# Kernel optimization log

Hardware: AMD Instinct MI355X
Metric: run time of the kernel (lower is better)

The kernel has to match this reference:

```python
import jax, jax.numpy as jnp
import numpy as np

INF_NUMBER = 1.0e12
ZERO_TOL = 1e-9
NEG_SLOPE = 0.2

B, G, N = 16, 128, 512
P, E, K, F = 4, 1, 3, 128


def setup_inputs() -> dict:
    key = jax.random.key(0)
    k1, k2, k3, k4, k5, k6, k7 = jax.random.split(key, 7)
    x = jax.random.normal(k1, (B, G, N), dtype=jnp.float32)
    u = jax.random.uniform(k2, (B, E, N, N), dtype=jnp.float32)
    S = jnp.where(u < 0.1, u, 0.0)
    std = 1.0 / np.sqrt(G * P)
    W = jax.random.uniform(k3, (P, E, G, G), minval=-std, maxval=std, dtype=jnp.float32)
    mixer = jax.random.uniform(k4, (P, E, 2 * F), minval=-std, maxval=std, dtype=jnp.float32)
    h = jax.random.uniform(k5, (P, F, E, K, G), minval=-std, maxval=std, dtype=jnp.float32)
    b = jax.random.uniform(k6, (F, 1), minval=-std, maxval=std, dtype=jnp.float32)
    return {"x": x, "S": S, "W": W, "mixer": mixer, "h": h, "b": b}


def _attention_gso(x, W, S):
    # x: (B,G,N); W: (P,E,G,G); S: (B,E,N,N)
    # Wx = W @ x_query : (B,P,E,G,N)
    Wx = jnp.einsum('pegh,bhn->bpegn', W, x)
    # xWx = x_key @ Wx : (B,P,E,N,N)  (x_key[b,m,g] = x[b,g,m])
    xWx = jnp.einsum('bgm,bpegn->bpemn', x, Wx)
    eij = jax.nn.leaky_relu(xWx, negative_slope=NEG_SLOPE)
    # edge mask from |S| summed over edge features: (B,1,1,N,N)
    mask = (jnp.sum(jnp.abs(S), axis=1) > ZERO_TOL).astype(x.dtype)[:, None, None]
    scores = eij * mask - (1.0 - mask) * INF_NUMBER
    aij = jax.nn.softmax(scores, axis=-1) * mask
    return aij  # (B,P,E,N,N)


def reference(x, S, W, mixer, h, b):
    # mixer is declared by the torch module but unused in key-query mode
    aij = _attention_gso(x, W, S)  # (B,P,E,N,N)
    # K-hop taps: z[k] = x @ aij^k, broadcast over (P,E)
    xk = jnp.broadcast_to(x[:, None, None], (B, P, E, G, N))
    taps = [xk]
    for _ in range(1, K):
        xk = jnp.einsum('bpegn,bpenm->bpegm', xk, aij)
        taps.append(xk)
    z = jnp.stack(taps, axis=3)  # (B,P,E,K,G,N)
    # filter GEMM: contract over (E,K,G) -> (B,P,F,N)
    y = jnp.einsum('bpekgn,pfekg->bpfn', z, h) + b  # b: (F,1) broadcasts
    # concatenate heads: relu then (B, P*F, N)
    y = jax.nn.relu(y)
    y = jnp.transpose(y, (0, 3, 1, 2)).reshape(B, N, P * F)
    return jnp.transpose(y, (0, 2, 1))
```

## Files before the change

### kernel.cpp

```cpp
#include <hip/hip_runtime.h>

#define Bx 16
#define Gx 128
#define Nx 512
#define Px 4
#define Kx 3
#define Fx 128
#define NEG_SLOPE 0.2f
#define ZERO_TOL 1e-9f
#define BIGF 1.0e30f

typedef unsigned short u16;
typedef unsigned int u32;
typedef __bf16 v8bf __attribute__((ext_vector_type(8)));
typedef _Float16 v8hf __attribute__((ext_vector_type(8)));
typedef float v4f __attribute__((ext_vector_type(4)));

__device__ __forceinline__ u16 f2b(float f) {
  union { float f; u32 u; } v; v.f = f;
  u32 r = (v.u + 0x7fffu + ((v.u >> 16) & 1u)) >> 16;
  return (u16)r;
}
__device__ __forceinline__ u16 f2h(float f) {
  union { _Float16 h; u16 u; } v; v.h = (_Float16)f;
  return v.u;
}

#define G2L16(gsrc, ldst)                                                     \
  __builtin_amdgcn_global_load_lds(                                           \
      (const __attribute__((address_space(1))) void*)(gsrc),                  \
      (__attribute__((address_space(3))) void*)(ldst), 16, 0, 0)

__global__ __launch_bounds__(256) void prep_kernel(const float* __restrict__ S,
                                                   const float* __restrict__ x,
                                                   const float* __restrict__ W,
                                                   const float* __restrict__ h,
                                                   u32* __restrict__ mb,
                                                   u16* __restrict__ xb,
                                                   u16* __restrict__ xTb,
                                                   u16* __restrict__ xT16,
                                                   u16* __restrict__ w16,
                                                   u16* __restrict__ Hb) {
  const int blk = blockIdx.x;
  const int tid = threadIdx.x;
  __shared__ float t[32][33];
  if (blk < 512) {
    const int wi = blk * 256 + tid;
    const float4* S4 = (const float4*)S;
    u32 bits = 0;
#pragma unroll
    for (int q = 0; q < 8; q++) {
      float4 v = S4[(size_t)wi * 8 + q];
      bits |= (fabsf(v.x) > ZERO_TOL ? 1u : 0u) << (q * 4);
      bits |= (fabsf(v.y) > ZERO_TOL ? 2u : 0u) << (q * 4);
      bits |= (fabsf(v.z) > ZERO_TOL ? 4u : 0u) << (q * 4);
      bits |= (fabsf(v.w) > ZERO_TOL ? 8u : 0u) << (q * 4);
    }
    mb[wi] = bits;
  } else if (blk < 1536) {
    const int idx = blk - 512;
    const int b = idx >> 6, g0 = ((idx >> 4) & 3) * 32, n0 = (idx & 15) * 32;
    const int r = tid >> 3, c4 = (tid & 7) * 4;
    const float* xp = x + (size_t)b * Gx * Nx;
    float4 v = *(const float4*)&xp[(g0 + r) * Nx + n0 + c4];
    ushort4 o;
    o.x = f2b(v.x); o.y = f2b(v.y); o.z = f2b(v.z); o.w = f2b(v.w);
    *(ushort4*)&xb[(size_t)b * Gx * Nx + (g0 + r) * Nx + n0 + c4] = o;
    t[r][c4 + 0] = v.x; t[r][c4 + 1] = v.y; t[r][c4 + 2] = v.z; t[r][c4 + 3] = v.w;
    __syncthreads();
    float tv[4] = {t[c4 + 0][r], t[c4 + 1][r], t[c4 + 2][r], t[c4 + 3][r]};
    ushort4 ob, oh;
    ob.x = f2b(tv[0]); oh.x = f2h(tv[0]);
    ob.y = f2b(tv[1]); oh.y = f2h(tv[1]);
    ob.z = f2b(tv[2]); oh.z = f2h(tv[2]);
    ob.w = f2b(tv[3]); oh.w = f2h(tv[3]);
    size_t off = (size_t)b * Nx * Gx + (size_t)(n0 + r) * Gx + g0 + c4;
    *(ushort4*)&xTb[off] = ob;
    *(ushort4*)&xT16[off] = oh;
  } else if (blk < 1600) {
    int i4 = ((blk - 1536) * 256 + tid) * 4;
    float4 v = *(const float4*)&W[i4];
    ushort4 o;
    o.x = f2h(v.x); o.y = f2h(v.y); o.z = f2h(v.z); o.w = f2h(v.w);
    *(ushort4*)&w16[i4] = o;
  } else {
    int i4 = ((blk - 1600) * 256 + tid) * 4;
    float4 v = *(const float4*)&h[i4];
    ushort4 o;
    o.x = f2b(v.x); o.y = f2b(v.y); o.z = f2b(v.z); o.w = f2b(v.w);
    *(ushort4*)&Hb[i4] = o;
  }
}

__global__ __launch_bounds__(256) void wxt16_kernel(const u16* __restrict__ xT16,
                                                    const u16* __restrict__ w16,
                                                    u16* __restrict__ WxT16) {
  __shared__ __align__(16) char smem[49152];
  constexpr int OB = 16384;
  const int bp = blockIdx.x, b = bp >> 2, p = bp & 3;
  const int rt = blockIdx.y;
  const int tid = threadIdx.x;
  const int w = tid >> 6, l = tid & 63;
  const int wr = w >> 1, wc = w & 1;
  const int lr = l & 15, ks = l >> 4;

  const u16* Ap = xT16 + ((size_t)b * Nx + rt * 64) * Gx;
  const u16* Bp = w16 + (size_t)p * Gx * Gx;
#pragma unroll
  for (int it = 0; it < 4; it++) {
    int chunk = it * 256 + w * 64 + l;
    int r = chunk >> 4, kq = l & 15;
    int kg = (kq ^ (r & 15)) * 8;
    G2L16(Ap + (size_t)r * Gx + kg, smem + it * 4096 + w * 1024);
  }
#pragma unroll
  for (int it = 0; it < 8; it++) {
    int chunk = it * 256 + w * 64 + l;
    int r = chunk >> 4, kq = l & 15;
    int kg = (kq ^ (r & 15)) * 8;
    G2L16(Bp + (size_t)r * Gx + kg, smem + OB + it * 4096 + w * 1024);
  }
  __syncthreads();

  v4f acc[2][4];
#pragma unroll
  for (int fr = 0; fr < 2; fr++)
#pragma unroll
    for (int fc = 0; fc < 4; fc++) acc[fr][fc] = (v4f){0.f, 0.f, 0.f, 0.f};

#pragma unroll
  for (int t = 0; t < 4; t++) {
    int kk = t * 4 + ks;
    v8hf ah[2];
#pragma unroll
    for (int fr = 0; fr < 2; fr++) {
      int ra = wr * 32 + fr * 16 + lr;
      ah[fr] = *(const v8hf*)(smem + ra * 256 + ((kk ^ (ra & 15)) * 16));
    }
#pragma unroll
    for (int fc = 0; fc < 4; fc++) {
      int rb = wc * 64 + fc * 16 + lr;
      v8hf bh = *(const v8hf*)(smem + OB + rb * 256 + ((kk ^ (rb & 15)) * 16));
#pragma unroll
      for (int fr = 0; fr < 2; fr++)
        acc[fr][fc] = __builtin_amdgcn_mfma_f32_16x16x32_f16(ah[fr], bh, acc[fr][fc], 0, 0, 0);
    }
  }

  u16* op = WxT16 + (size_t)bp * Nx * Gx;
#pragma unroll
  for (int fr = 0; fr < 2; fr++)
#pragma unroll
    for (int fc = 0; fc < 4; fc++) {
      int n = rt * 64 + wr * 32 + fr * 16 + ks * 4;
      int g = wc * 64 + fc * 16 + lr;
#pragma unroll
      for (int q = 0; q < 4; q++) op[(size_t)(n + q) * Gx + g] = f2h(acc[fr][fc][q]);
    }
}

__global__ __launch_bounds__(512) void attn4_kernel(const u16* __restrict__ xT16,
                                                    const u16* __restrict__ WxT16,
                                                    const u32* __restrict__ mb,
                                                    u16* __restrict__ aijT) {
  __shared__ __align__(16) char smem[55296];
  constexpr int OB = 16384, OMBS = 49152, ORED = 53248;
  const int bp = blockIdx.x, b = bp >> 2;
  const int i0 = blockIdx.y * 64;
  const int tid = threadIdx.x;
  const int w = tid >> 6, l = tid & 63;
  const int wr = w >> 2, wc = w & 3;
  const int lr = l & 15, ks = l >> 4;

  {
    const u32* mbp = mb + ((size_t)b * Nx + i0) * 16;
    u32* mbs = (u32*)(smem + OMBS);
    mbs[tid] = mbp[tid];
    mbs[tid + 512] = mbp[tid + 512];
  }
  {
    const u16* Ap = xT16 + ((size_t)b * Nx + i0) * Gx;
#pragma unroll
    for (int it = 0; it < 2; it++) {
      int chunk = it * 512 + w * 64 + l;
      int r = chunk >> 4, kq = l & 15;
      int kg = (kq ^ (r & 15)) * 8;
      G2L16(Ap + (size_t)r * Gx + kg, smem + it * 8192 + w * 1024);
    }
  }

  v4f acc[2][8];
#pragma unroll
  for (int fr = 0; fr < 2; fr++)
#pragma unroll
    for (int fc = 0; fc < 8; fc++) acc[fr][fc] = (v4f){0.f, 0.f, 0.f, 0.f};

  const u16* Bp = WxT16 + (size_t)bp * Nx * Gx;
  for (int g0 = 0; g0 < Gx; g0 += 32) {
    __syncthreads();
#pragma unroll
    for (int it = 0; it < 4; it++) {
      int chunk = it * 512 + w * 64 + l;
      int r = chunk >> 2, kq = l & 3;
      int kg = (kq ^ (r & 3)) * 8;
      G2L16(Bp + (size_t)r * Gx + g0 + kg, smem + OB + it * 8192 + w * 1024);
    }
    __syncthreads();
    int kk = (g0 >> 3) + ks;
    v8hf ah[2];
#pragma unroll
    for (int fr = 0; fr < 2; fr++) {
      int ra = wr * 32 + fr * 16 + lr;
      ah[fr] = *(const v8hf*)(smem + ra * 256 + ((kk ^ (ra & 15)) * 16));
    }
#pragma unroll
    for (int fc = 0; fc < 8; fc++) {
      int rb = wc * 128 + fc * 16 + lr;
      v8hf bh = *(const v8hf*)(smem + OB + rb * 64 + ((ks ^ (rb & 3)) * 16));
#pragma unroll
      for (int fr = 0; fr < 2; fr++)
        acc[fr][fc] = __builtin_amdgcn_mfma_f32_16x16x32_f16(ah[fr], bh, acc[fr][fc], 0, 0, 0);
    }
  }

  u32* mbs = (u32*)(smem + OMBS);
  float* red0 = (float*)(smem + ORED);
  float* red1 = red0 + 256;

#pragma unroll
  for (int fr = 0; fr < 2; fr++)
#pragma unroll
    for (int q = 0; q < 4; q++) {
      int row = wr * 32 + fr * 16 + ks * 4 + q;
      float m = -BIGF;
#pragma unroll
      for (int fc = 0; fc < 8; fc++) {
        u32 word = mbs[row * 16 + wc * 4 + (fc >> 1)];
        int bit = ((fc & 1) << 4) + lr;
        float v = acc[fr][fc][q];
        v = v >= 0.f ? v : NEG_SLOPE * v;
        v = ((word >> bit) & 1u) ? v : -BIGF;
        acc[fr][fc][q] = v;
        m = fmaxf(m, v);
      }
      m = fmaxf(m, __shfl_xor(m, 1, 64));
      m = fmaxf(m, __shfl_xor(m, 2, 64));
      m = fmaxf(m, __shfl_xor(m, 4, 64));
      m = fmaxf(m, __shfl_xor(m, 8, 64));
      if (lr == 0) red0[row * 4 + wc] = m;
    }
  __syncthreads();
#pragma unroll
  for (int fr = 0; fr < 2; fr++)
#pragma unroll
    for (int q = 0; q < 4; q++) {
      int row = wr * 32 + fr * 16 + ks * 4 + q;
      float4 pm = *(const float4*)&red0[row * 4];
      float gm = fmaxf(fmaxf(pm.x, pm.y), fmaxf(pm.z, pm.w));
      float s = 0.f;
#pragma unroll
      for (int fc = 0; fc < 8; fc++) {
        float v = acc[fr][fc][q];
        float e = (v <= -0.5f * BIGF) ? 0.f : __expf(v - gm);
        acc[fr][fc][q] = e;
        s += e;
      }
      s += __shfl_xor(s, 1, 64);
      s += __shfl_xor(s, 2, 64);
      s += __shfl_xor(s, 4, 64);
      s += __shfl_xor(s, 8, 64);
      if (lr == 0) red1[row * 4 + wc] = s;
    }
  __syncthreads();
  u16* dst = aijT + (size_t)bp * Nx * Nx + i0;
#pragma unroll
  for (int fr = 0; fr < 2; fr++) {
    int rbase = wr * 32 + fr * 16 + ks * 4;
    float inv[4];
#pragma unroll
    for (int q = 0; q < 4; q++) {
      float4 ps = *(const float4*)&red1[(rbase + q) * 4];
      float tot = (ps.x + ps.y) + (ps.z + ps.w);
      inv[q] = tot > 0.f ? 1.f / tot : 0.f;
    }
#pragma unroll
    for (int fc = 0; fc < 8; fc++) {
      int j = wc * 128 + fc * 16 + lr;
      ushort4 pk;
      pk.x = f2b(acc[fr][fc][0] * inv[0]);
      pk.y = f2b(acc[fr][fc][1] * inv[1]);
      pk.z = f2b(acc[fr][fc][2] * inv[2]);
      pk.w = f2b(acc[fr][fc][3] * inv[3]);
      *(ushort4*)&dst[(size_t)j * Nx + rbase] = pk;
    }
  }
}

template <int MODE>
__global__ __launch_bounds__(256) void gnt_kernel(const u16* __restrict__ pA,
                                                  const u16* __restrict__ pB,
                                                  const u16* __restrict__ pC,
                                                  const u16* __restrict__ pHb,
                                                  u16* __restrict__ o1,
                                                  u16* __restrict__ o2,
                                                  float* __restrict__ oF,
                                                  const float* __restrict__ bias) {
  __shared__ __align__(16) char smem[2][12288];
  const int bp = blockIdx.x;
  const int b = bp >> 2, p = bp & 3;
  const int by = blockIdx.y;
  const int rt = (MODE == 1) ? (by >> 2) : by;
  const int ct = (MODE == 1) ? (by & 3) : 0;
  const int tid = threadIdx.x;
  const int w = tid >> 6, l = tid & 63;
  const int wr = w >> 1, wc = w & 1;
  const int lr = l & 15, kslot = l >> 4;

  constexpr int KTOT = (MODE == 2) ? (Kx * Gx) : Nx;
  constexpr int SA = (MODE == 2) ? Gx : Nx;
  constexpr int SB = (MODE == 2) ? (Kx * Gx) : Nx;
  constexpr int NT = KTOT / 32;

  const u16* Abase;
  const u16* Bbase;
  if (MODE == 0) {
    Abase = pA + (size_t)bp * Nx * Nx + (size_t)rt * 64 * Nx;
    Bbase = pB + (size_t)b * Gx * Nx;
  } else if (MODE == 1) {
    Abase = pA + (size_t)bp * Gx * Nx + (size_t)rt * 64 * Nx;
    Bbase = pB + (size_t)bp * Nx * Nx + (size_t)ct * 128 * Nx;
  } else {
    Abase = nullptr;
    Bbase = pHb + (size_t)p * Fx * (Kx * Gx);
  }

  const int sar = tid >> 2;
  const int sakg = (tid & 3) ^ (sar & 3);
  const int sbr0 = tid >> 2, sbkg0 = (tid & 3) ^ (sbr0 & 3);
  const int sbr1 = (tid + 256) >> 2, sbkg1 = (tid & 3) ^ (sbr1 & 3);

  int aoff[2], boff[4];
#pragma unroll
  for (int fr = 0; fr < 2; fr++) {
    int row = wr * 32 + fr * 16 + lr;
    aoff[fr] = row * 64 + ((kslot ^ (row & 3)) * 16);
  }
#pragma unroll
  for (int fc = 0; fc < 4; fc++) {
    int row = wc * 64 + fc * 16 + lr;
    boff[fc] = 4096 + row * 64 + ((kslot ^ (row & 3)) * 16);
  }

  auto STAGE = [&](int bufi, int k0) {
    const u16* Aseg;
    int kin;
    if (MODE == 2) {
      int seg = k0 >> 7;
      kin = k0 & 127;
      const u16* base = (seg == 0) ? (pA + (size_t)b * Nx * Gx)
                       : (seg == 1) ? (pB + (size_t)bp * Nx * Gx)
                                    : (pC + (size_t)bp * Nx * Gx);
      Aseg = base + (size_t)rt * 64 * Gx;
    } else {
      Aseg = Abase;
      kin = k0;
    }
    char* base = smem[bufi];
    G2L16(Aseg + (size_t)sar * SA + kin + sakg * 8, base + w * 1024);
    G2L16(Bbase + (size_t)sbr0 * SB + k0 + sbkg0 * 8, base + 4096 + w * 1024);
    G2L16(Bbase + (size_t)sbr1 * SB + k0 + sbkg1 * 8, base + 8192 + w * 1024);
  };

  v4f acc[2][4];
#pragma unroll
  for (int fr = 0; fr < 2; fr++)
#pragma unroll
    for (int fc = 0; fc < 4; fc++) acc[fr][fc] = (v4f){0.f, 0.f, 0.f, 0.f};

  STAGE(0, 0);
  int cur = 0;
  for (int t = 0; t < NT; t++) {
    __syncthreads();
    if (t + 1 < NT) STAGE(cur ^ 1, (t + 1) * 32);
    const char* bb = smem[cur];
    v8bf af[2], bf4[4];
#pragma unroll
    for (int fr = 0; fr < 2; fr++) af[fr] = *(const v8bf*)(bb + aoff[fr]);
#pragma unroll
    for (int fc = 0; fc < 4; fc++) bf4[fc] = *(const v8bf*)(bb + boff[fc]);
#pragma unroll
    for (int fr = 0; fr < 2; fr++)
#pragma unroll
      for (int fc = 0; fc < 4; fc++)
        acc[fr][fc] = __builtin_amdgcn_mfma_f32_16x16x32_bf16(af[fr], bf4[fc],
                                                              acc[fr][fc], 0, 0, 0);
    cur ^= 1;
  }

  if (MODE == 0) {
    u16* z1p = o1 + (size_t)bp * Gx * Nx;
    u16* z1Tp = o2 + (size_t)bp * Nx * Gx;
#pragma unroll
    for (int fr = 0; fr < 2; fr++)
#pragma unroll
      for (int fc = 0; fc < 4; fc++) {
        int m0 = rt * 64 + wr * 32 + fr * 16 + kslot * 4;
        int g = wc * 64 + fc * 16 + lr;
        v4f a = acc[fr][fc];
        ushort4 pk;
        pk.x = f2b(a[0]); pk.y = f2b(a[1]); pk.z = f2b(a[2]); pk.w = f2b(a[3]);
        *(ushort4*)&z1p[(size_t)g * Nx + m0] = pk;
        z1Tp[(size_t)(m0 + 0) * Gx + g] = pk.x;
        z1Tp[(size_t)(m0 + 1) * Gx + g] = pk.y;
        z1Tp[(size_t)(m0 + 2) * Gx + g] = pk.z;
        z1Tp[(size_t)(m0 + 3) * Gx + g] = pk.w;
      }
  } else if (MODE == 1) {
    u16* z2Tp = o1 + (size_t)bp * Nx * Gx;
#pragma unroll
    for (int fr = 0; fr < 2; fr++)
#pragma unroll
      for (int fc = 0; fc < 4; fc++) {
        int g0r = rt * 64 + wr * 32 + fr * 16 + kslot * 4;
        int m = ct * 128 + wc * 64 + fc * 16 + lr;
        v4f a = acc[fr][fc];
        ushort4 pk;
        pk.x = f2b(a[0]); pk.y = f2b(a[1]); pk.z = f2b(a[2]); pk.w = f2b(a[3]);
        *(ushort4*)&z2Tp[(size_t)m * Gx + g0r] = pk;
      }
  } else {
    float* op = oF + (size_t)(b * Px + p) * Fx * Nx;
#pragma unroll
    for (int fc = 0; fc < 4; fc++) {
      int f = wc * 64 + fc * 16 + lr;
      float bi = bias[f];
#pragma unroll
      for (int fr = 0; fr < 2; fr++) {
        int n0 = rt * 64 + wr * 32 + fr * 16 + kslot * 4;
        v4f a = acc[fr][fc];
        float4 o;
        o.x = fmaxf(a[0] + bi, 0.f);
        o.y = fmaxf(a[1] + bi, 0.f);
        o.z = fmaxf(a[2] + bi, 0.f);
        o.w = fmaxf(a[3] + bi, 0.f);
        *(float4*)&op[(size_t)f * Nx + n0] = o;
      }
    }
  }
}

extern "C" void kernel_launch(void* const* d_in, const int* in_sizes, int n_in,
                              void* d_out, int out_size, void* d_ws, size_t ws_size,
                              hipStream_t stream) {
  const float* x = (const float*)d_in[0];
  const float* S = (const float*)d_in[1];
  const float* W = (const float*)d_in[2];
  const float* h = (const float*)d_in[4];
  const float* bias = (const float*)d_in[5];
  float* out = (float*)d_out;

  char* ws = (char*)d_ws;
  u16* aijT  = (u16*)ws;
  u16* WxT16 = (u16*)(ws + 33554432);
  u16* xT16  = (u16*)(ws + 41943040);
  u16* xTb   = (u16*)(ws + 44040192);
  u16* xb    = (u16*)(ws + 46137344);
  u16* z1    = (u16*)(ws + 48234496);
  u16* z1T   = (u16*)(ws + 56623104);
  u16* z2T   = (u16*)(ws + 65011712);
  u16* Hb    = (u16*)(ws + 73400320);
  u16* W16   = (u16*)(ws + 73793536);
  u32* mb    = (u32*)(ws + 73924608);

  prep_kernel<<<dim3(1792), 256, 0, stream>>>(S, x, W, h, mb, xb, xTb, xT16, W16, Hb);
  wxt16_kernel<<<dim3(Bx * Px, Nx / 64), 256, 0, stream>>>(xT16, W16, WxT16);
  attn4_kernel<<<dim3(Bx * Px, Nx / 64), 512, 0, stream>>>(xT16, WxT16, mb, aijT);
  gnt_kernel<0><<<dim3(Bx * Px, 8), 256, 0, stream>>>(aijT, xb, nullptr, nullptr,
                                                      z1, z1T, nullptr, nullptr);
  gnt_kernel<1><<<dim3(Bx * Px, 8), 256, 0, stream>>>(z1, aijT, nullptr, nullptr,
                                                      z2T, nullptr, nullptr, nullptr);
  gnt_kernel<2><<<dim3(Bx * Px, 8), 256, 0, stream>>>(xTb, z1T, z2T, Hb,
                                                      nullptr, nullptr, out, bias);
  (void)in_sizes; (void)n_in; (void)out_size; (void)ws_size;
}
```

Before: 77.14 us.

## Double-buffer WxT tiles and preload A fragments into registers in attention kernel

The attention score kernel now loads all A (x) fragments into registers up front, which frees that shared memory. The K-loop uses two 32KB shared buffers so the next WxT tile is issued while MFMAs run on the current one. This removes one barrier per iteration and lets global loads overlap compute. In exchange it raises shared memory to about 70KB per block and adds launch_bounds(512,4), which may hurt occupancy or cause register spills.

Result: slower. 78.82 us (+2.2%).

```diff
diff --git a/kernel.cpp b/kernel.cpp
--- a/kernel.cpp
+++ b/kernel.cpp
@@ -159,12 +159,12 @@
     }
 }
 
-__global__ __launch_bounds__(512) void attn4_kernel(const u16* __restrict__ xT16,
-                                                    const u16* __restrict__ WxT16,
-                                                    const u32* __restrict__ mb,
-                                                    u16* __restrict__ aijT) {
-  __shared__ __align__(16) char smem[55296];
-  constexpr int OB = 16384, OMBS = 49152, ORED = 53248;
+__global__ __launch_bounds__(512, 4) void attn5_kernel(const u16* __restrict__ xT16,
+                                                       const u16* __restrict__ WxT16,
+                                                       const u32* __restrict__ mb,
+                                                       u16* __restrict__ aijT) {
+  __shared__ __align__(16) char smem[71680];
+  constexpr int OMBS = 65536, ORED = 69632;
   const int bp = blockIdx.x, b = bp >> 2;
   const int i0 = blockIdx.y * 64;
   const int tid = threadIdx.x;
@@ -188,38 +188,51 @@
       G2L16(Ap + (size_t)r * Gx + kg, smem + it * 8192 + w * 1024);
     }
   }
-
-  v4f acc[2][8];
-#pragma unroll
-  for (int fr = 0; fr < 2; fr++)
-#pragma unroll
-    for (int fc = 0; fc < 8; fc++) acc[fr][fc] = (v4f){0.f, 0.f, 0.f, 0.f};
+  __syncthreads();
+
+  v8hf areg[2][4];
+#pragma unroll
+  for (int fr = 0; fr < 2; fr++) {
+    int ra = wr * 32 + fr * 16 + lr;
+#pragma unroll
+    for (int t = 0; t < 4; t++) {
+      int kk = t * 4 + ks;
+      areg[fr][t] = *(const v8hf*)(smem + ra * 256 + ((kk ^ (ra & 15)) * 16));
+    }
+  }
+  __syncthreads();
 
   const u16* Bp = WxT16 + (size_t)bp * Nx * Gx;
-  for (int g0 = 0; g0 < Gx; g0 += 32) {
-    __syncthreads();
+  auto STAGE_B = [&](int t) {
+    char* dst = smem + (t & 1) * 32768;
+    int g0 = t * 32;
 #pragma unroll
     for (int it = 0; it < 4; it++) {
       int chunk = it * 512 + w * 64 + l;
       int r = chunk >> 2, kq = l & 3;
       int kg = (kq ^ (r & 3)) * 8;
-      G2L16(Bp + (size_t)r * Gx + g0 + kg, smem + OB + it * 8192 + w * 1024);
-    }
+      G2L16(Bp + (size_t)r * Gx + g0 + kg, dst + it * 8192 + w * 1024);
+    }
+  };
+
+  v4f acc[2][8];
+#pragma unroll
+  for (int fr = 0; fr < 2; fr++)
+#pragma unroll
+    for (int fc = 0; fc < 8; fc++) acc[fr][fc] = (v4f){0.f, 0.f, 0.f, 0.f};
+
+  STAGE_B(0);
+  for (int t = 0; t < 4; t++) {
     __syncthreads();
-    int kk = (g0 >> 3) + ks;
-    v8hf ah[2];
-#pragma unroll
-    for (int fr = 0; fr < 2; fr++) {
-      int ra = wr * 32 + fr * 16 + lr;
-      ah[fr] = *(const v8hf*)(smem + ra * 256 + ((kk ^ (ra & 15)) * 16));
-    }
+    if (t < 3) STAGE_B(t + 1);
+    const char* bb = smem + (t & 1) * 32768;
 #pragma unroll
     for (int fc = 0; fc < 8; fc++) {
       int rb = wc * 128 + fc * 16 + lr;
-      v8hf bh = *(const v8hf*)(smem + OB + rb * 64 + ((ks ^ (rb & 3)) * 16));
+      v8hf bh = *(const v8hf*)(bb + rb * 64 + ((ks ^ (rb & 3)) * 16));
 #pragma unroll
       for (int fr = 0; fr < 2; fr++)
-        acc[fr][fc] = __builtin_amdgcn_mfma_f32_16x16x32_f16(ah[fr], bh, acc[fr][fc], 0, 0, 0);
+        acc[fr][fc] = __builtin_amdgcn_mfma_f32_16x16x32_f16(areg[fr][t], bh, acc[fr][fc], 0, 0, 0);
     }
   }
 
@@ -474,7 +487,7 @@
 
   prep_kernel<<<dim3(1792), 256, 0, stream>>>(S, x, W, h, mb, xb, xTb, xT16, W16, Hb);
   wxt16_kernel<<<dim3(Bx * Px, Nx / 64), 256, 0, stream>>>(xT16, W16, WxT16);
-  attn4_kernel<<<dim3(Bx * Px, Nx / 64), 512, 0, stream>>>(xT16, WxT16, mb, aijT);
+  attn5_kernel<<<dim3(Bx * Px, Nx / 64), 512, 0, stream>>>(xT16, WxT16, mb, aijT);
   gnt_kernel<0><<<dim3(Bx * Px, 8), 256, 0, stream>>>(aijT, xb, nullptr, nullptr,
                                                       z1, z1T, nullptr, nullptr);
   gnt_kernel<1><<<dim3(Bx * Px, 8), 256, 0, stream>>>(z1, aijT, nullptr, nullptr,
```
